# Optimization experiments

Measured on AMD Instinct MI355X. Metric: run time of the kernel, lower is better.

The kernel has to match this reference:

```python
import jax, jax.numpy as jnp
import numpy as np
from jax.ops import segment_sum, segment_max

N, F_IN, HID, HEADS, NCLS, E = 50000, 256, 64, 8, 16, 400000
NEG_SLOPE = 0.2


def setup_inputs() -> dict:
    key = jax.random.key(0)
    ks = jax.random.split(key, 10)
    x = jax.random.normal(ks[0], (N, F_IN), dtype=jnp.float32)
    edge_index = jax.random.randint(ks[1], (2, E), 0, N, dtype=jnp.int64)
    s1 = 1.0 / np.sqrt(F_IN)
    s2 = 1.0 / np.sqrt(HID * HEADS)
    return {
        "x": x,
        "edge_index": edge_index,
        "W1": jax.random.normal(ks[2], (F_IN, HEADS * HID), dtype=jnp.float32) * s1,
        "a_src1": jax.random.normal(ks[3], (HEADS, HID), dtype=jnp.float32) * 0.1,
        "a_dst1": jax.random.normal(ks[4], (HEADS, HID), dtype=jnp.float32) * 0.1,
        "b1": jnp.zeros((HEADS * HID,), dtype=jnp.float32),
        "W2": jax.random.normal(ks[5], (HEADS * HID, NCLS), dtype=jnp.float32) * s2,
        "a_src2": jax.random.normal(ks[6], (1, NCLS), dtype=jnp.float32) * 0.1,
        "a_dst2": jax.random.normal(ks[7], (1, NCLS), dtype=jnp.float32) * 0.1,
        "b2": jnp.zeros((NCLS,), dtype=jnp.float32),
    }


def _gat_conv(x, src, dst, W, a_src, a_dst, bias, heads, out_c, concat):
    n = x.shape[0]
    h = (x @ W).reshape(n, heads, out_c)          # [N, H, C]
    # per-node attention halves (PyG trick: dot before gather)
    al_src = jnp.einsum('nhc,hc->nh', h, a_src)    # [N, H]
    al_dst = jnp.einsum('nhc,hc->nh', h, a_dst)    # [N, H]
    alpha = al_src[src] + al_dst[dst]              # [E, H]
    alpha = jax.nn.leaky_relu(alpha, NEG_SLOPE)
    # segment softmax over destination neighborhoods
    m = segment_max(alpha, dst, num_segments=n)
    ex = jnp.exp(alpha - m[dst])
    denom = segment_sum(ex, dst, num_segments=n)
    alpha = ex / denom[dst]                        # [E, H]
    msg = h[src] * alpha[:, :, None]               # [E, H, C]
    out = segment_sum(msg, dst, num_segments=n)    # [N, H, C]
    if concat:
        out = out.reshape(n, heads * out_c)
    else:
        out = out.mean(axis=1)
    return out + bias


def reference(x, edge_index, W1, a_src1, a_dst1, b1, W2, a_src2, a_dst2, b2):
    n = x.shape[0]
    # PyG GATConv default: add self-loops
    loop = jnp.arange(n, dtype=edge_index.dtype)
    src = jnp.concatenate([edge_index[0], loop])
    dst = jnp.concatenate([edge_index[1], loop])
    h = _gat_conv(x, src, dst, W1, a_src1, a_dst1, b1, HEADS, HID, True)
    h = jax.nn.elu(h)
    # dropout layers are identity in eval mode
    out = _gat_conv(h, src, dst, W2, a_src2, a_dst2, b2, 1, NCLS, False)
    return out
```

## Files before the change

kernel.cpp:

```cpp
#include <hip/hip_runtime.h>
#include <hip/hip_bf16.h>
#include <math.h>

#define N_NODES 50000
#define F_INK   256
#define HEADS   8
#define HID     64
#define HH      512
#define NCLS    16
#define NEDGE   400000
#define NEG_SLOPE 0.2f

#define BCOLS 64
#define KPAD  264
#define NBLK_SCAN ((N_NODES + 255) / 256)
#define X2ROW 584
#define X2GB  72

typedef __attribute__((ext_vector_type(8))) short short8;
typedef __attribute__((ext_vector_type(4))) short sh4;
typedef __attribute__((ext_vector_type(4))) float float4v;

__device__ __forceinline__ float bf2f(unsigned short u){
    unsigned int x = ((unsigned int)u) << 16;
    float f; __builtin_memcpy(&f, &x, 4); return f;
}
__device__ __forceinline__ unsigned short f2bf(float f){
    unsigned int x; __builtin_memcpy(&x, &f, 4);
    unsigned int r = x + 0x7FFFu + ((x >> 16) & 1u);
    return (unsigned short)(r >> 16);
}
__device__ __forceinline__ float lrelu(float a){ return a > 0.f ? a : NEG_SLOPE * a; }

__device__ __forceinline__ void fma8(float* acc, float w, short8 v){
    unsigned int u[4]; __builtin_memcpy(u, &v, 16);
#pragma unroll
    for (int j = 0; j < 4; j++){
        acc[2*j]   += w * __uint_as_float(u[j] << 16);
        acc[2*j+1] += w * __uint_as_float(u[j] & 0xffff0000u);
    }
}

__global__ void cvt_f32_bf16(const float* __restrict__ in, unsigned short* __restrict__ out, int n4){
    int i = blockIdx.x * blockDim.x + threadIdx.x;
    int stride = gridDim.x * blockDim.x;
    for (; i < n4; i += stride){
        float4v f = *(const float4v*)(in + (size_t)i * 4);
        sh4 o;
#pragma unroll
        for (int j = 0; j < 4; j++) o[j] = (short)f2bf(f[j]);
        *(sh4*)(out + (size_t)i * 4) = o;
    }
}

__global__ void cvt_weights(const float* __restrict__ W1, unsigned short* __restrict__ W1T,
                            const float* __restrict__ W2, unsigned short* __restrict__ W2T){
    int i = blockIdx.x * blockDim.x + threadIdx.x;
    if (i < F_INK * HH){
        int k = i / HH, c = i % HH;
        W1T[c * F_INK + k] = f2bf(W1[i]);
    }
    int j = i - F_INK * HH;
    if (j >= 0 && j < HH * NCLS){
        int k = j / NCLS, c = j % NCLS;
        W2T[c * HH + k] = f2bf(W2[j]);
    }
}

__global__ void count_edges(const int* __restrict__ dst, int* __restrict__ counts,
                            int* __restrict__ erank){
    int e = blockIdx.x * blockDim.x + threadIdx.x;
    if (e < NEDGE) erank[e] = atomicAdd(&counts[dst[e]], 1);
}

__global__ __launch_bounds__(256) void scan_part(const int* __restrict__ counts,
                                                 int* __restrict__ blocksums){
    __shared__ int red[256];
    int i = blockIdx.x * 256 + threadIdx.x;
    int v = (i < N_NODES) ? counts[i] : 0;
    red[threadIdx.x] = v; __syncthreads();
    for (int off = 128; off > 0; off >>= 1){
        if (threadIdx.x < off) red[threadIdx.x] += red[threadIdx.x + off];
        __syncthreads();
    }
    if (threadIdx.x == 0) blocksums[blockIdx.x] = red[0];
}

__global__ __launch_bounds__(256) void scan_top(const int* __restrict__ blocksums,
                                                int* __restrict__ blockbase,
                                                int* __restrict__ offsets){
    __shared__ int s[256];
    int t = threadIdx.x;
    int v = (t < NBLK_SCAN) ? blocksums[t] : 0;
    s[t] = v; __syncthreads();
    int val = v;
    for (int off = 1; off < 256; off <<= 1){
        int o2 = (t >= off) ? s[t - off] : 0;
        __syncthreads();
        val += o2; s[t] = val;
        __syncthreads();
    }
    if (t < NBLK_SCAN) blockbase[t] = val - v;
    if (t == 255) offsets[N_NODES] = s[255];
}

__global__ __launch_bounds__(256) void scan_write(const int* __restrict__ counts,
                                                  const int* __restrict__ blockbase,
                                                  int* __restrict__ offsets){
    __shared__ int s[256];
    int i = blockIdx.x * 256 + threadIdx.x;
    int t = threadIdx.x;
    int v = (i < N_NODES) ? counts[i] : 0;
    s[t] = v; __syncthreads();
    int val = v;
    for (int off = 1; off < 256; off <<= 1){
        int o2 = (t >= off) ? s[t - off] : 0;
        __syncthreads();
        val += o2; s[t] = val;
        __syncthreads();
    }
    if (i < N_NODES) offsets[i] = blockbase[blockIdx.x] + val - v;
}

__global__ void scatter_edges(const int* __restrict__ src, const int* __restrict__ dst,
                              const int* __restrict__ offsets, const int* __restrict__ erank,
                              int* __restrict__ esrc){
    int e = blockIdx.x * blockDim.x + threadIdx.x;
    if (e < NEDGE) esrc[offsets[dst[e]] + erank[e]] = src[e];
}

__global__ __launch_bounds__(256) void gemm1(const unsigned short* __restrict__ xb,
                                             const unsigned short* __restrict__ w1t,
                                             const float* __restrict__ a_src,
                                             const float* __restrict__ a_dst,
                                             unsigned short* __restrict__ h1b,
                                             float* __restrict__ al_s,
                                             float* __restrict__ al_d){
    __shared__ unsigned short bs[BCOLS * KPAD];
    int cb  = blockIdx.x & 7;
    int rg  = blockIdx.x >> 3;
    int nrg = gridDim.x >> 3;
    {
        int kc = threadIdx.x & 31;
        int c0 = threadIdx.x >> 5;
#pragma unroll
        for (int it = 0; it < 8; it++){
            int col = it * 8 + c0;
            short8 v = *(const short8*)(w1t + (size_t)(cb * BCOLS + col) * F_INK + kc * 8);
            *(short8*)(&bs[col * KPAD + kc * 8]) = v;
        }
    }
    __syncthreads();
    int w    = threadIdx.x >> 6;
    int lane = threadIdx.x & 63;
    int lr = lane & 15, lk = lane >> 4;
    float a_s[4], a_d[4];
#pragma unroll
    for (int ct = 0; ct < 4; ct++){
        a_s[ct] = a_src[cb * HID + ct * 16 + lr];
        a_d[ct] = a_dst[cb * HID + ct * 16 + lr];
    }
    const int nchunk = (N_NODES + 127) / 128;
    for (int ch = rg; ch < nchunk; ch += nrg){
        int rb0 = ch * 128 + w * 32;
        if (rb0 >= N_NODES) continue;
        bool t1 = (rb0 + 16 < N_NODES);
        short8 a0[8], a1[8];
#pragma unroll
        for (int ks = 0; ks < 8; ks++)
            a0[ks] = *(const short8*)(xb + (size_t)(rb0 + lr) * F_INK + ks * 32 + lk * 8);
        if (t1){
#pragma unroll
            for (int ks = 0; ks < 8; ks++)
                a1[ks] = *(const short8*)(xb + (size_t)(rb0 + 16 + lr) * F_INK + ks * 32 + lk * 8);
        }
        float ds0[4] = {0.f,0.f,0.f,0.f}, dd0[4] = {0.f,0.f,0.f,0.f};
        float ds1[4] = {0.f,0.f,0.f,0.f}, dd1[4] = {0.f,0.f,0.f,0.f};
#pragma unroll
        for (int ct = 0; ct < 4; ct++){
            float4v acc0 = {0.f, 0.f, 0.f, 0.f};
            float4v acc1 = {0.f, 0.f, 0.f, 0.f};
#pragma unroll
            for (int ks = 0; ks < 8; ks++){
                short8 b = *(const short8*)(&bs[(ct * 16 + lr) * KPAD + ks * 32 + lk * 8]);
                acc0 = __builtin_amdgcn_mfma_f32_16x16x32_bf16(a0[ks], b, acc0, 0, 0, 0);
                if (t1) acc1 = __builtin_amdgcn_mfma_f32_16x16x32_bf16(a1[ks], b, acc1, 0, 0, 0);
            }
#pragma unroll
            for (int r = 0; r < 4; r++){
                h1b[(size_t)(rb0 + lk * 4 + r) * HH + cb * BCOLS + ct * 16 + lr] = f2bf(acc0[r]);
                ds0[r] += acc0[r] * a_s[ct];
                dd0[r] += acc0[r] * a_d[ct];
            }
            if (t1){
#pragma unroll
                for (int r = 0; r < 4; r++){
                    h1b[(size_t)(rb0 + 16 + lk * 4 + r) * HH + cb * BCOLS + ct * 16 + lr] = f2bf(acc1[r]);
                    ds1[r] += acc1[r] * a_s[ct];
                    dd1[r] += acc1[r] * a_d[ct];
                }
            }
        }
#pragma unroll
        for (int r = 0; r < 4; r++){
#pragma unroll
            for (int o = 1; o < 16; o <<= 1){
                ds0[r] += __shfl_xor(ds0[r], o);
                dd0[r] += __shfl_xor(dd0[r], o);
                ds1[r] += __shfl_xor(ds1[r], o);
                dd1[r] += __shfl_xor(dd1[r], o);
            }
        }
        if (lr == 0){
#pragma unroll
            for (int r = 0; r < 4; r++){
                al_s[(rb0 + lk * 4 + r) * HEADS + cb] = ds0[r];
                al_d[(rb0 + lk * 4 + r) * HEADS + cb] = dd0[r];
            }
            if (t1){
#pragma unroll
                for (int r = 0; r < 4; r++){
                    al_s[(rb0 + 16 + lk * 4 + r) * HEADS + cb] = ds1[r];
                    al_d[(rb0 + 16 + lk * 4 + r) * HEADS + cb] = dd1[r];
                }
            }
        }
    }
}

__global__ __launch_bounds__(256) void softmax1(
        const float* __restrict__ al_s, const float* __restrict__ al_d,
        const int* __restrict__ offsets, const int* __restrict__ esrc,
        float* __restrict__ ew, float* __restrict__ wselfr, float* __restrict__ dinv){
    int d = blockIdx.x * 4 + (threadIdx.x >> 6);
    int lane = threadIdx.x & 63;
    if (d >= N_NODES) return;
    int h = lane & 7, i = lane >> 3;
    int off = offsets[d], deg = offsets[d + 1] - off;
    float ald = al_d[d * HEADS + h];
    float aself = lrelu(al_s[d * HEADS + h] + ald);
    float m = aself;
    for (int base = 0; base < deg; base += 8){
        int e = base + i;
        float a = -1e30f;
        if (e < deg) a = lrelu(al_s[esrc[off + e] * HEADS + h] + ald);
        a = fmaxf(a, __shfl_xor(a, 8));
        a = fmaxf(a, __shfl_xor(a, 16));
        a = fmaxf(a, __shfl_xor(a, 32));
        m = fmaxf(m, a);
    }
    float denom = __expf(aself - m);
    for (int base = 0; base < deg; base += 8){
        int e = base + i;
        float w = 0.f;
        if (e < deg){
            w = __expf(lrelu(al_s[esrc[off + e] * HEADS + h] + ald) - m);
            ew[(size_t)(off + e) * HEADS + h] = w;
        }
        float ws = w;
        ws += __shfl_xor(ws, 8);
        ws += __shfl_xor(ws, 16);
        ws += __shfl_xor(ws, 32);
        denom += ws;
    }
    if (i == 0){
        wselfr[d * HEADS + h] = __expf(aself - m);
        dinv[d * HEADS + h]   = 1.f / denom;
    }
}

__global__ __launch_bounds__(256) void agg1f(const unsigned short* __restrict__ h1b,
        const float* __restrict__ ew, const float* __restrict__ wselfr,
        const float* __restrict__ dinv,
        const int* __restrict__ offsets, const int* __restrict__ esrc,
        const float* __restrict__ b1,
        const unsigned short* __restrict__ w2t,
        const float* __restrict__ a_s2, const float* __restrict__ a_d2,
        float* __restrict__ h2, float* __restrict__ al2s, float* __restrict__ al2d){
    __shared__ unsigned short x2l[16 * X2ROW];
    int w = threadIdx.x >> 6;
    int lane = threadIdx.x & 63;
    int g = lane >> 3, i = lane & 7;
    int cb = g * HID + i * 8;
#pragma unroll
    for (int q = 0; q < 4; q++){
        int row = w * 4 + q;
        int d = blockIdx.x * 16 + row;
        int off = offsets[d], deg = offsets[d + 1] - off;
        float acc[8];
        {
            float w0 = wselfr[d * HEADS + g];
            short8 v = *(const short8*)(h1b + (size_t)d * HH + cb);
            unsigned int u[4]; __builtin_memcpy(u, &v, 16);
#pragma unroll
            for (int j = 0; j < 4; j++){
                acc[2*j]   = w0 * __uint_as_float(u[j] << 16);
                acc[2*j+1] = w0 * __uint_as_float(u[j] & 0xffff0000u);
            }
        }
        int e = 0;
        for (; e + 4 <= deg; e += 4){
            int s0 = __builtin_amdgcn_readfirstlane(esrc[off + e]);
            int s1 = __builtin_amdgcn_readfirstlane(esrc[off + e + 1]);
            int s2 = __builtin_amdgcn_readfirstlane(esrc[off + e + 2]);
            int s3 = __builtin_amdgcn_readfirstlane(esrc[off + e + 3]);
            float w0 = ew[(size_t)(off + e)     * HEADS + g];
            float w1 = ew[(size_t)(off + e + 1) * HEADS + g];
            float w2 = ew[(size_t)(off + e + 2) * HEADS + g];
            float w3 = ew[(size_t)(off + e + 3) * HEADS + g];
            short8 v0 = *(const short8*)(h1b + (size_t)s0 * HH + cb);
            short8 v1 = *(const short8*)(h1b + (size_t)s1 * HH + cb);
            short8 v2 = *(const short8*)(h1b + (size_t)s2 * HH + cb);
            short8 v3 = *(const short8*)(h1b + (size_t)s3 * HH + cb);
            fma8(acc, w0, v0); fma8(acc, w1, v1);
            fma8(acc, w2, v2); fma8(acc, w3, v3);
        }
        for (; e < deg; e++){
            int s0 = __builtin_amdgcn_readfirstlane(esrc[off + e]);
            float w0 = ew[(size_t)(off + e) * HEADS + g];
            short8 v0 = *(const short8*)(h1b + (size_t)s0 * HH + cb);
            fma8(acc, w0, v0);
        }
        float di = dinv[d * HEADS + g];
        unsigned short o8[8];
#pragma unroll
        for (int j = 0; j < 8; j++){
            float v = acc[j] * di + b1[cb + j];
            v = v > 0.f ? v : __expf(v) - 1.f;
            o8[j] = f2bf(v);
        }
        short8 ov; __builtin_memcpy(&ov, o8, 16);
        *(short8*)(&x2l[row * X2ROW + g * X2GB + i * 8]) = ov;
    }
    __syncthreads();
    if (w == 0){
        int rowbase = blockIdx.x * 16;
        int lr = lane & 15, lk = lane >> 4;
        float4v accv = {0.f, 0.f, 0.f, 0.f};
#pragma unroll
        for (int ks = 0; ks < 16; ks++){
            int c0 = ks * 32 + lk * 8;
            int gg = c0 >> 6, wc = c0 & 63;
            short8 a = *(const short8*)(&x2l[lr * X2ROW + gg * X2GB + wc]);
            short8 b = *(const short8*)(w2t + (size_t)lr * HH + ks * 32 + lk * 8);
            accv = __builtin_amdgcn_mfma_f32_16x16x32_bf16(a, b, accv, 0, 0, 0);
        }
#pragma unroll
        for (int r = 0; r < 4; r++)
            h2[(size_t)(rowbase + lk * 4 + r) * NCLS + lr] = accv[r];
        float s_a = a_s2[lr], d_a = a_d2[lr];
#pragma unroll
        for (int r = 0; r < 4; r++){
            float ps = accv[r] * s_a, pd = accv[r] * d_a;
#pragma unroll
            for (int off = 1; off < 16; off <<= 1){
                ps += __shfl_xor(ps, off);
                pd += __shfl_xor(pd, off);
            }
            if (lr == 0){
                al2s[rowbase + lk * 4 + r] = ps;
                al2d[rowbase + lk * 4 + r] = pd;
            }
        }
    }
}

__global__ __launch_bounds__(256) void agg2(const float* __restrict__ h2,
        const float* __restrict__ al2s, const float* __restrict__ al2d,
        const int* __restrict__ offsets, const int* __restrict__ esrc,
        const float* __restrict__ b2, float* __restrict__ out){
    int d = blockIdx.x * 4 + (threadIdx.x >> 6);
    int lane = threadIdx.x & 63;
    if (d >= N_NODES) return;
    int off = offsets[d], deg = offsets[d + 1] - off;
    float ald = al2d[d];
    float a0 = lrelu(al2s[d] + ald);
    float m = a0;
    for (int base = 0; base < deg; base += 64){
        int e = base + lane;
        float a = (e < deg) ? lrelu(al2s[esrc[off + e]] + ald) : -1e30f;
#pragma unroll
        for (int o = 1; o < 64; o <<= 1) a = fmaxf(a, __shfl_xor(a, o));
        m = fmaxf(m, a);
    }
    float dsum = __expf(a0 - m);
    for (int base = 0; base < deg; base += 64){
        int e = base + lane;
        float w = (e < deg) ? __expf(lrelu(al2s[esrc[off + e]] + ald) - m) : 0.f;
#pragma unroll
        for (int o = 1; o < 64; o <<= 1) w += __shfl_xor(w, o);
        dsum += w;
    }
    int sg = lane >> 4, col = lane & 15;
    float acc = (sg == 0) ? __expf(a0 - m) * h2[(size_t)d * NCLS + col] : 0.f;
    for (int i = sg; i < deg; i += 4){
        int s = esrc[off + i];
        float w = __expf(lrelu(al2s[s] + ald) - m);
        acc += w * h2[(size_t)s * NCLS + col];
    }
    acc += __shfl_xor(acc, 16);
    acc += __shfl_xor(acc, 32);
    if (lane < NCLS) out[(size_t)d * NCLS + lane] = acc / dsum + b2[lane];
}

extern "C" void kernel_launch(void* const* d_in, const int* in_sizes, int n_in,
                              void* d_out, int out_size, void* d_ws, size_t ws_size,
                              hipStream_t stream){
    const float* x   = (const float*)d_in[0];
    const int*   ei  = (const int*)d_in[1];
    const int*   src = ei;
    const int*   dst = ei + NEDGE;
    const float* W1  = (const float*)d_in[2];
    const float* as1 = (const float*)d_in[3];
    const float* ad1 = (const float*)d_in[4];
    const float* b1  = (const float*)d_in[5];
    const float* W2  = (const float*)d_in[6];
    const float* as2 = (const float*)d_in[7];
    const float* ad2 = (const float*)d_in[8];
    const float* b2  = (const float*)d_in[9];
    float* out = (float*)d_out;

    char* p = (char*)d_ws;
    auto carve = [&](size_t bytes) -> char* {
        char* r = p; p += (bytes + 255) & ~(size_t)255; return r;
    };
    unsigned short* xb   = (unsigned short*)carve((size_t)N_NODES * F_INK * 2);
    unsigned short* w1t  = (unsigned short*)carve((size_t)HH * F_INK * 2);
    unsigned short* w2t  = (unsigned short*)carve((size_t)HH * NCLS * 2);
    unsigned short* h1b  = (unsigned short*)carve((size_t)N_NODES * HH * 2);
    float* al1s  = (float*)carve((size_t)N_NODES * HEADS * 4);
    float* al1d  = (float*)carve((size_t)N_NODES * HEADS * 4);
    int* counts  = (int*)carve((size_t)N_NODES * 4);
    int* erank   = (int*)carve((size_t)NEDGE * 4);
    int* offsets = (int*)carve((size_t)(N_NODES + 1) * 4);
    int* blocksums = (int*)carve((size_t)NBLK_SCAN * 4);
    int* blockbase = (int*)carve((size_t)NBLK_SCAN * 4);
    int* esrc    = (int*)carve((size_t)NEDGE * 4);
    float* ew    = (float*)carve((size_t)NEDGE * HEADS * 4);
    float* wselfr= (float*)carve((size_t)N_NODES * HEADS * 4);
    float* dinv  = (float*)carve((size_t)N_NODES * HEADS * 4);
    float* h2    = (float*)carve((size_t)N_NODES * NCLS * 4);
    float* al2s  = (float*)carve((size_t)N_NODES * 4);
    float* al2d  = (float*)carve((size_t)N_NODES * 4);
    if ((size_t)(p - (char*)d_ws) > ws_size) return;

    hipMemsetAsync(counts, 0, N_NODES * 4, stream);

    cvt_f32_bf16<<<2048, 256, 0, stream>>>(x, xb, N_NODES * F_INK / 4);
    cvt_weights<<<(F_INK * HH + HH * NCLS + 255) / 256, 256, 0, stream>>>(W1, w1t, W2, w2t);
    count_edges<<<(NEDGE + 255) / 256, 256, 0, stream>>>(dst, counts, erank);
    scan_part<<<NBLK_SCAN, 256, 0, stream>>>(counts, blocksums);
    scan_top<<<1, 256, 0, stream>>>(blocksums, blockbase, offsets);
    scan_write<<<NBLK_SCAN, 256, 0, stream>>>(counts, blockbase, offsets);
    scatter_edges<<<(NEDGE + 255) / 256, 256, 0, stream>>>(src, dst, offsets, erank, esrc);
    gemm1<<<8 * 128, 256, 0, stream>>>(xb, w1t, as1, ad1, h1b, al1s, al1d);
    softmax1<<<(N_NODES + 3) / 4, 256, 0, stream>>>(al1s, al1d, offsets, esrc, ew, wselfr, dinv);
    agg1f<<<N_NODES / 16, 256, 0, stream>>>(h1b, ew, wselfr, dinv, offsets, esrc, b1,
                                            w2t, as2, ad2, h2, al2s, al2d);
    agg2<<<(N_NODES + 3) / 4, 256, 0, stream>>>(h2, al2s, al2d, offsets, esrc, b2, out);
}
```

Before: 234.8 us.

## Merge prep kernels, fuse edge scatter into GEMM launch, single-pass agg2 for small degree

Folds the x conversion, weight transposes and edge counting into one launch using block-index ranges, and appends the edge-scatter blocks to the gemm1 grid. This removes several kernel launches and lets independent work run side by side. agg2 gains a fast path for nodes with degree up to 64: attention logits are loaded once into registers and reused through shuffles for max, sum and weighting, instead of being recomputed in three passes. Costs are a larger gemm1 grid whose scatter blocks still reserve shared memory, and more branching code in agg2.

```diff
diff --git a/kernel.cpp b/kernel.cpp
--- a/kernel.cpp
+++ b/kernel.cpp
@@ -16,6 +16,10 @@
 #define NBLK_SCAN ((N_NODES + 255) / 256)
 #define X2ROW 584
 #define X2GB  72
+#define PREP_X_BLKS 12500
+#define PREP_W_BLKS 544
+#define G1_BLKS 1024
+#define SCAT_BLKS ((NEDGE + 255) / 256)
 
 typedef __attribute__((ext_vector_type(8))) short short8;
 typedef __attribute__((ext_vector_type(4))) short sh4;
@@ -41,36 +45,33 @@
     }
 }
 
-__global__ void cvt_f32_bf16(const float* __restrict__ in, unsigned short* __restrict__ out, int n4){
-    int i = blockIdx.x * blockDim.x + threadIdx.x;
-    int stride = gridDim.x * blockDim.x;
-    for (; i < n4; i += stride){
-        float4v f = *(const float4v*)(in + (size_t)i * 4);
+__global__ __launch_bounds__(256) void prep(const float* __restrict__ x, unsigned short* __restrict__ xb,
+                                            const float* __restrict__ W1, unsigned short* __restrict__ W1T,
+                                            const float* __restrict__ W2, unsigned short* __restrict__ W2T,
+                                            const int* __restrict__ dst, int* __restrict__ counts,
+                                            int* __restrict__ erank){
+    int bid = blockIdx.x;
+    if (bid < PREP_X_BLKS){
+        int i = bid * 256 + threadIdx.x;
+        float4v f = *(const float4v*)(x + (size_t)i * 4);
         sh4 o;
 #pragma unroll
         for (int j = 0; j < 4; j++) o[j] = (short)f2bf(f[j]);
-        *(sh4*)(out + (size_t)i * 4) = o;
-    }
-}
-
-__global__ void cvt_weights(const float* __restrict__ W1, unsigned short* __restrict__ W1T,
-                            const float* __restrict__ W2, unsigned short* __restrict__ W2T){
-    int i = blockIdx.x * blockDim.x + threadIdx.x;
-    if (i < F_INK * HH){
-        int k = i / HH, c = i % HH;
-        W1T[c * F_INK + k] = f2bf(W1[i]);
-    }
-    int j = i - F_INK * HH;
-    if (j >= 0 && j < HH * NCLS){
-        int k = j / NCLS, c = j % NCLS;
-        W2T[c * HH + k] = f2bf(W2[j]);
-    }
-}
-
-__global__ void count_edges(const int* __restrict__ dst, int* __restrict__ counts,
-                            int* __restrict__ erank){
-    int e = blockIdx.x * blockDim.x + threadIdx.x;
-    if (e < NEDGE) erank[e] = atomicAdd(&counts[dst[e]], 1);
+        *(sh4*)(xb + (size_t)i * 4) = o;
+    } else if (bid < PREP_X_BLKS + PREP_W_BLKS){
+        int i = (bid - PREP_X_BLKS) * 256 + threadIdx.x;
+        if (i < F_INK * HH){
+            int k = i / HH, c = i % HH;
+            W1T[c * F_INK + k] = f2bf(W1[i]);
+        } else {
+            int j = i - F_INK * HH;
+            int k = j / NCLS, c = j % NCLS;
+            W2T[c * HH + k] = f2bf(W2[j]);
+        }
+    } else {
+        int e = (bid - PREP_X_BLKS - PREP_W_BLKS) * 256 + threadIdx.x;
+        if (e < NEDGE) erank[e] = atomicAdd(&counts[dst[e]], 1);
+    }
 }
 
 __global__ __launch_bounds__(256) void scan_part(const int* __restrict__ counts,
@@ -122,24 +123,22 @@
     if (i < N_NODES) offsets[i] = blockbase[blockIdx.x] + val - v;
 }
 
-__global__ void scatter_edges(const int* __restrict__ src, const int* __restrict__ dst,
-                              const int* __restrict__ offsets, const int* __restrict__ erank,
-                              int* __restrict__ esrc){
-    int e = blockIdx.x * blockDim.x + threadIdx.x;
-    if (e < NEDGE) esrc[offsets[dst[e]] + erank[e]] = src[e];
-}
-
-__global__ __launch_bounds__(256) void gemm1(const unsigned short* __restrict__ xb,
-                                             const unsigned short* __restrict__ w1t,
-                                             const float* __restrict__ a_src,
-                                             const float* __restrict__ a_dst,
-                                             unsigned short* __restrict__ h1b,
-                                             float* __restrict__ al_s,
-                                             float* __restrict__ al_d){
+__global__ __launch_bounds__(256) void gemm1_scatter(
+        const unsigned short* __restrict__ xb, const unsigned short* __restrict__ w1t,
+        const float* __restrict__ a_src, const float* __restrict__ a_dst,
+        unsigned short* __restrict__ h1b, float* __restrict__ al_s, float* __restrict__ al_d,
+        const int* __restrict__ src, const int* __restrict__ dst,
+        const int* __restrict__ offsets, const int* __restrict__ erank,
+        int* __restrict__ esrc){
     __shared__ unsigned short bs[BCOLS * KPAD];
+    if (blockIdx.x >= G1_BLKS){
+        int e = (blockIdx.x - G1_BLKS) * 256 + threadIdx.x;
+        if (e < NEDGE) esrc[offsets[dst[e]] + erank[e]] = src[e];
+        return;
+    }
     int cb  = blockIdx.x & 7;
     int rg  = blockIdx.x >> 3;
-    int nrg = gridDim.x >> 3;
+    const int nrg = G1_BLKS >> 3;
     {
         int kc = threadIdx.x & 31;
         int c0 = threadIdx.x >> 5;
@@ -375,28 +374,48 @@
     int off = offsets[d], deg = offsets[d + 1] - off;
     float ald = al2d[d];
     float a0 = lrelu(al2s[d] + ald);
-    float m = a0;
-    for (int base = 0; base < deg; base += 64){
-        int e = base + lane;
-        float a = (e < deg) ? lrelu(al2s[esrc[off + e]] + ald) : -1e30f;
-#pragma unroll
-        for (int o = 1; o < 64; o <<= 1) a = fmaxf(a, __shfl_xor(a, o));
-        m = fmaxf(m, a);
-    }
-    float dsum = __expf(a0 - m);
-    for (int base = 0; base < deg; base += 64){
-        int e = base + lane;
-        float w = (e < deg) ? __expf(lrelu(al2s[esrc[off + e]] + ald) - m) : 0.f;
-#pragma unroll
-        for (int o = 1; o < 64; o <<= 1) w += __shfl_xor(w, o);
-        dsum += w;
-    }
     int sg = lane >> 4, col = lane & 15;
-    float acc = (sg == 0) ? __expf(a0 - m) * h2[(size_t)d * NCLS + col] : 0.f;
-    for (int i = sg; i < deg; i += 4){
-        int s = esrc[off + i];
-        float w = __expf(lrelu(al2s[s] + ald) - m);
-        acc += w * h2[(size_t)s * NCLS + col];
+    float m, dsum, acc;
+    if (deg <= 64){
+        float ae = -1e30f;
+        if (lane < deg) ae = lrelu(al2s[esrc[off + lane]] + ald);
+        float t = fmaxf(ae, a0);
+#pragma unroll
+        for (int o = 1; o < 64; o <<= 1) t = fmaxf(t, __shfl_xor(t, o));
+        m = t;
+        float ws = (lane < deg) ? __expf(ae - m) : 0.f;
+#pragma unroll
+        for (int o = 1; o < 64; o <<= 1) ws += __shfl_xor(ws, o);
+        dsum = ws + __expf(a0 - m);
+        acc = (sg == 0) ? __expf(a0 - m) * h2[(size_t)d * NCLS + col] : 0.f;
+        for (int i = sg; i < deg; i += 4){
+            int s = esrc[off + i];
+            float ai = __shfl(ae, i);
+            acc += __expf(ai - m) * h2[(size_t)s * NCLS + col];
+        }
+    } else {
+        m = a0;
+        for (int base = 0; base < deg; base += 64){
+            int e = base + lane;
+            float a = (e < deg) ? lrelu(al2s[esrc[off + e]] + ald) : -1e30f;
+#pragma unroll
+            for (int o = 1; o < 64; o <<= 1) a = fmaxf(a, __shfl_xor(a, o));
+            m = fmaxf(m, a);
+        }
+        dsum = __expf(a0 - m);
+        for (int base = 0; base < deg; base += 64){
+            int e = base + lane;
+            float w = (e < deg) ? __expf(lrelu(al2s[esrc[off + e]] + ald) - m) : 0.f;
+#pragma unroll
+            for (int o = 1; o < 64; o <<= 1) w += __shfl_xor(w, o);
+            dsum += w;
+        }
+        acc = (sg == 0) ? __expf(a0 - m) * h2[(size_t)d * NCLS + col] : 0.f;
+        for (int i = sg; i < deg; i += 4){
+            int s = esrc[off + i];
+            float w = __expf(lrelu(al2s[s] + ald) - m);
+            acc += w * h2[(size_t)s * NCLS + col];
+        }
     }
     acc += __shfl_xor(acc, 16);
     acc += __shfl_xor(acc, 32);
@@ -446,14 +465,13 @@
 
     hipMemsetAsync(counts, 0, N_NODES * 4, stream);
 
-    cvt_f32_bf16<<<2048, 256, 0, stream>>>(x, xb, N_NODES * F_INK / 4);
-    cvt_weights<<<(F_INK * HH + HH * NCLS + 255) / 256, 256, 0, stream>>>(W1, w1t, W2, w2t);
-    count_edges<<<(NEDGE + 255) / 256, 256, 0, stream>>>(dst, counts, erank);
+    prep<<<PREP_X_BLKS + PREP_W_BLKS + SCAT_BLKS, 256, 0, stream>>>(
+        x, xb, W1, w1t, W2, w2t, dst, counts, erank);
     scan_part<<<NBLK_SCAN, 256, 0, stream>>>(counts, blocksums);
     scan_top<<<1, 256, 0, stream>>>(blocksums, blockbase, offsets);
     scan_write<<<NBLK_SCAN, 256, 0, stream>>>(counts, blockbase, offsets);
-    scatter_edges<<<(NEDGE + 255) / 256, 256, 0, stream>>>(src, dst, offsets, erank, esrc);
-    gemm1<<<8 * 128, 256, 0, stream>>>(xb, w1t, as1, ad1, h1b, al1s, al1d);
+    gemm1_scatter<<<G1_BLKS + SCAT_BLKS, 256, 0, stream>>>(
+        xb, w1t, as1, ad1, h1b, al1s, al1d, src, dst, offsets, erank, esrc);
     softmax1<<<(N_NODES + 3) / 4, 256, 0, stream>>>(al1s, al1d, offsets, esrc, ew, wselfr, dinv);
     agg1f<<<N_NODES / 16, 256, 0, stream>>>(h1b, ew, wselfr, dinv, offsets, esrc, b1,
                                             w2t, as2, ad2, h2, al2s, al2d);
```

Measured after the change: 221.6 us. 1.06x faster.
